# Kernel tuning notes

Hardware: AMD Instinct MI355X
Metric: run time of the kernel (lower is better)

## Reference

```python
import jax, jax.numpy as jnp
import numpy as np

PC_MIN = jnp.array([0.0, -40.0, -3.0], dtype=jnp.float32)
VS_TOP = jnp.array([0.4, 0.4, 4.0], dtype=jnp.float32)
VS_MED = jnp.array([0.2, 0.2, 2.0], dtype=jnp.float32)
VS_LOW = jnp.array([0.1, 0.1, 1.0], dtype=jnp.float32)
GRID_TOP = (176, 200, 1)
GRID_MED = (352, 400, 2)
GRID_LOW = (704, 800, 4)
EPS = 1e-3
FILL = np.iinfo(np.int32).max


def _bn(x, g, b):
    # training-mode BatchNorm1d over the point/voxel axis (naiveSyncBN1d, eps=1e-3)
    mu = jnp.mean(x, axis=0)
    var = jnp.var(x, axis=0)
    return (x - mu) * jax.lax.rsqrt(var + EPS) * g + b


def _decode(lin, gx, gy, gz):
    x = lin % gx
    r = lin // gx
    y = r % gy
    r = r // gy
    z = r % gz
    b = r // gz
    return b, x, y, z


def _vfe(pts, batch, vs, grid, W1, g1, b1, W2, g2, b2):
    # Dynamic voxelization + DynamicScatterVFE (cluster center + voxel center, 2 layers, scatter-mean).
    N = pts.shape[0]
    gx, gy, gz = grid
    xyz = pts[:, :3]
    coors = jnp.floor((xyz - PC_MIN) / vs).astype(jnp.int32)
    cx = jnp.clip(coors[:, 0], 0, gx - 1)
    cy = jnp.clip(coors[:, 1], 0, gy - 1)
    cz = jnp.clip(coors[:, 2], 0, gz - 1)
    lin = ((batch * gz + cz) * gy + cy) * gx + cx  # linear voxel id incl. batch
    uniq, inv = jnp.unique(lin, return_inverse=True, size=N, fill_value=FILL)
    valid = uniq != FILL
    cnt = jnp.maximum(jax.ops.segment_sum(jnp.ones((N,), pts.dtype), inv, num_segments=N), 1.0)
    seg_mean = lambda v: jax.ops.segment_sum(v, inv, num_segments=N) / cnt[:, None]
    f_cluster = xyz - seg_mean(xyz)[inv]                      # offset from per-voxel point mean
    centers = PC_MIN + (jnp.stack([cx, cy, cz], axis=1).astype(pts.dtype) + 0.5) * vs
    f_center = xyz - centers                                   # offset from voxel center
    feats = jnp.concatenate([pts, f_cluster, f_center], axis=1)  # [N, 10]
    h = jax.nn.relu(_bn(feats @ W1, g1, b1))
    h = jnp.concatenate([h, seg_mean(h)[inv]], axis=1)           # point feat || gathered voxel feat
    h = jax.nn.relu(_bn(h @ W2, g2, b2))
    vox = seg_mean(h)
    return jnp.where(valid[:, None], vox, 0.0), uniq, valid


def _merge(sub_feats, sub_uniq, sub_valid, top_uniq, sub_grid, factor):
    # find_coordinate_indices + scatter_v2(mode='avg'): mean of child voxel feats per parent voxel.
    b, x, y, z = _decode(sub_uniq, *sub_grid)
    gx, gy, gz = GRID_TOP
    parent = ((b * gz + z // factor) * gy + y // factor) * gx + x // factor
    M = top_uniq.shape[0]
    pos = jnp.clip(jnp.searchsorted(top_uniq, parent), 0, M - 1)
    found = sub_valid & (top_uniq[pos] == parent)
    seg = jnp.where(found, pos, M)  # unmatched/padding rows dropped into slot M
    s = jax.ops.segment_sum(sub_feats, seg, num_segments=M + 1)[:M]
    c = jax.ops.segment_sum(found.astype(sub_feats.dtype), seg, num_segments=M + 1)[:M]
    return s / jnp.maximum(c, 1.0)[:, None]


def setup_inputs() -> dict:
    key = jax.random.key(0)
    ks = jax.random.split(key, 12)
    N, B = 262144, 2
    x = jax.random.uniform(ks[0], (N, 1), jnp.float32, 0.0, 70.4)
    y = jax.random.uniform(ks[1], (N, 1), jnp.float32, -40.0, 40.0)
    z = jax.random.uniform(ks[2], (N, 1), jnp.float32, -3.0, 1.0)
    inten = jax.random.uniform(ks[3], (N, 1), jnp.float32)
    bcol = jnp.repeat(jnp.arange(B, dtype=jnp.float32), N // B)[:, None]
    points = jnp.concatenate([bcol, x, y, z, inten], axis=1)
    lin_w = lambda k, i, o: jax.random.normal(k, (i, o), jnp.float32) * (1.0 / np.sqrt(i))
    return dict(
        points=points, batch_size=2,
        W1_top=lin_w(ks[4], 10, 64), g1_top=jnp.ones(64), b1_top=jnp.zeros(64),
        W2_top=lin_w(ks[5], 128, 128), g2_top=jnp.ones(128), b2_top=jnp.zeros(128),
        W1_med=lin_w(ks[6], 10, 32), g1_med=jnp.ones(32), b1_med=jnp.zeros(32),
        W2_med=lin_w(ks[7], 64, 64), g2_med=jnp.ones(64), b2_med=jnp.zeros(64),
        W1_low=lin_w(ks[8], 10, 32), g1_low=jnp.ones(32), b1_low=jnp.zeros(32),
        W2_low=lin_w(ks[9], 64, 64), g2_low=jnp.ones(64), b2_low=jnp.zeros(64),
    )


def reference(points, batch_size, W1_top, g1_top, b1_top, W2_top, g2_top, b2_top,
              W1_med, g1_med, b1_med, W2_med, g2_med, b2_med,
              W1_low, g1_low, b1_low, W2_low, g2_low, b2_low):
    batch = points[:, 0].astype(jnp.int32)
    pts = points[:, 1:]
    vf, top_uniq, top_valid = _vfe(pts, batch, VS_TOP, GRID_TOP, W1_top, g1_top, b1_top, W2_top, g2_top, b2_top)
    mfeat, med_uniq, med_valid = _vfe(pts, batch, VS_MED, GRID_MED, W1_med, g1_med, b1_med, W2_med, g2_med, b2_med)
    lfeat, low_uniq, low_valid = _vfe(pts, batch, VS_LOW, GRID_LOW, W1_low, g1_low, b1_low, W2_low, g2_low, b2_low)
    med_mean = _merge(mfeat, med_uniq, med_valid, top_uniq, GRID_MED, 2)
    low_mean = _merge(lfeat, low_uniq, low_valid, top_uniq, GRID_LOW, 4)
    merged = jnp.where(top_valid[:, None], jnp.concatenate([med_mean, low_mean], axis=1), 0.0)
    b, x, y, z = _decode(top_uniq, *GRID_TOP)
    coors = jnp.where(top_valid[:, None], jnp.stack([b, z, y, x], axis=1), -1)
    return vf, merged, coors
```

## Files before the change

### kernel.cpp

```cpp
#include <hip/hip_runtime.h>
#include <cstdint>
#include <cstddef>

#define NPTS 262144
#define BLK 256
#define TGX 176
#define TGY 200
#define TGZ 1

#define G_TOPC 70400
#define G_MEDC 1126400
#define G_LOWC 4505600

#define SCAN_ITEMS 32
#define SCAN_CHUNK (BLK*SCAN_ITEMS)
#define NB_T 9
#define NB_M 138
#define NB_L 550
#define BO_T 0
#define BO_M 16
#define BO_L 160
#define NBVT (G_TOPC/BLK)
#define NBVM (NPTS/BLK)
#define NBVL (NPTS/BLK)

#define Y2B2 (NPTS/64)
#define ST1BLKS 256
#define NHT 4400
#define NHM 8192
#define NJT 8800
#define NJM 16384
#define NCL 275

typedef __attribute__((ext_vector_type(8))) short bf16x8;
typedef __attribute__((ext_vector_type(4))) float f32x4;

struct SP {
  const float4* srt; const int* jr; const float4* vm;
  const float* W1; const float* W2;
  const float* g1; const float* b1; const float* g2; const float* b2;
  const int* cnt; const int* uniq; const int* woff; const int* U;
  float* segt; float* part1; float* part2;
  float* coef1; float* coef2;
  unsigned short* Y2;
  float* hout;
  int C1; int segstride; int gx, gy, gz; float vx, vy, vz;
};

__device__ __forceinline__ unsigned short f2bf(float v) {
  unsigned u = __float_as_uint(v);
  u += 0x7FFFu + ((u >> 16) & 1u);
  return (unsigned short)(u >> 16);
}
__device__ __forceinline__ float bf2f(unsigned short h) {
  return __uint_as_float((unsigned)h << 16);
}

__device__ __forceinline__ void pcoords(float x, float y, float z,
    float vx, float vy, float vz, int gx, int gy, int gz,
    int& cx, int& cy, int& cz) {
  cx = (int)floorf((x - 0.0f)  / vx);
  cy = (int)floorf((y + 40.0f) / vy);
  cz = (int)floorf((z + 3.0f)  / vz);
  cx = min(max(cx, 0), gx - 1);
  cy = min(max(cy, 0), gy - 1);
  cz = min(max(cz, 0), gz - 1);
}

__device__ __forceinline__ int lin3(float b, float x, float y, float z,
    float vx, float vy, float vz, int gx, int gy, int gz) {
  int cx, cy, cz; pcoords(x, y, z, vx, vy, vz, gx, gy, gz, cx, cy, cz);
  return (((int)b * gz + cz) * gy + cy) * gx + cx;
}

__device__ __forceinline__ void build_f(float4 p, float4 vm,
    float vx, float vy, float vz, int gx, int gy, int gz, float* f) {
  int cx, cy, cz; pcoords(p.x, p.y, p.z, vx, vy, vz, gx, gy, gz, cx, cy, cz);
  f[0] = p.x; f[1] = p.y; f[2] = p.z; f[3] = p.w;
  f[4] = p.x - vm.x;
  f[5] = p.y - vm.y;
  f[6] = p.z - vm.z;
  f[7] = p.x - (0.0f   + (cx + 0.5f)*vx);
  f[8] = p.y - (-40.0f + (cy + 0.5f)*vy);
  f[9] = p.z - (-3.0f  + (cz + 0.5f)*vz);
}

__global__ __launch_bounds__(BLK) void k_count3(const float* __restrict__ pts,
    int* __restrict__ ct, int* __restrict__ cm, int* __restrict__ cl) {
  int i = blockIdx.x * BLK + threadIdx.x;
  if (i >= NPTS) return;
  float b = pts[i*5+0], x = pts[i*5+1], y = pts[i*5+2], z = pts[i*5+3];
  atomicAdd(&ct[lin3(b,x,y,z, 0.4f,0.4f,4.0f, 176,200,1)], 1);
  atomicAdd(&cm[lin3(b,x,y,z, 0.2f,0.2f,2.0f, 352,400,2)], 1);
  atomicAdd(&cl[lin3(b,x,y,z, 0.1f,0.1f,1.0f, 704,800,4)], 1);
}

__global__ __launch_bounds__(BLK) void k_scan1_all(const int* __restrict__ ct,
    const int* __restrict__ cm, const int* __restrict__ cl,
    int2* __restrict__ bsum) {
  int bid = blockIdx.x;
  const int* cnt; int G, bo, cb;
  if (bid < NB_T)            { cnt = ct; G = G_TOPC; bo = BO_T; cb = bid; }
  else if (bid < NB_T+NB_M)  { cnt = cm; G = G_MEDC; bo = BO_M; cb = bid - NB_T; }
  else                       { cnt = cl; G = G_LOWC; bo = BO_L; cb = bid - NB_T - NB_M; }
  int base = cb * SCAN_CHUNK + threadIdx.x * SCAN_ITEMS;
  int so = 0, sp = 0;
  #pragma unroll
  for (int k = 0; k < SCAN_ITEMS; k++) {
    int j = base + k;
    if (j < G) { int c = cnt[j]; if (c > 0) { so++; sp += c; } }
  }
  __shared__ int sho[BLK], shp[BLK];
  sho[threadIdx.x] = so; shp[threadIdx.x] = sp; __syncthreads();
  for (int off = BLK/2; off > 0; off >>= 1) {
    if (threadIdx.x < off) {
      sho[threadIdx.x] += sho[threadIdx.x + off];
      shp[threadIdx.x] += shp[threadIdx.x + off];
    }
    __syncthreads();
  }
  if (threadIdx.x == 0) { int2 v; v.x = sho[0]; v.y = shp[0]; bsum[bo + cb] = v; }
}

__device__ void scan_pass(int2* bsum, int off, int nb, int* U,
                          int* so, int* sp) {
  int t = threadIdx.x;
  int vo = 0, vp = 0;
  if (t < nb) { int2 v = bsum[off + t]; vo = v.x; vp = v.y; }
  so[t] = vo; sp[t] = vp; __syncthreads();
  for (int o = 1; o < 1024; o <<= 1) {
    int ao = (t >= o) ? so[t - o] : 0;
    int ap = (t >= o) ? sp[t - o] : 0;
    __syncthreads();
    so[t] += ao; sp[t] += ap;
    __syncthreads();
  }
  if (t < nb) { int2 e; e.x = so[t] - vo; e.y = sp[t] - vp; bsum[off + t] = e; }
  if (t == 0) *U = so[1023];
  __syncthreads();
}

__global__ __launch_bounds__(1024) void k_scan2_all(int2* __restrict__ bsum,
    int* __restrict__ Ut, int* __restrict__ Um, int* __restrict__ Ul) {
  __shared__ int so[1024], sp[1024];
  scan_pass(bsum, BO_T, NB_T, Ut, so, sp);
  scan_pass(bsum, BO_M, NB_M, Um, so, sp);
  scan_pass(bsum, BO_L, NB_L, Ul, so, sp);
}

__global__ __launch_bounds__(BLK) void k_scan3_all(const int* __restrict__ ct,
    const int* __restrict__ cm, const int* __restrict__ cl,
    const int2* __restrict__ bsum,
    int* __restrict__ rkt, int* __restrict__ rkm, int* __restrict__ rkl,
    int* __restrict__ uqt, int* __restrict__ uqm, int* __restrict__ uql,
    int* __restrict__ wot, int* __restrict__ wom, int* __restrict__ wol) {
  int bid = blockIdx.x;
  const int* cnt; int G, bo, cb; int *rank, *uniq, *woff;
  if (bid < NB_T)           { cnt=ct; G=G_TOPC; bo=BO_T; cb=bid;            rank=rkt; uniq=uqt; woff=wot; }
  else if (bid < NB_T+NB_M) { cnt=cm; G=G_MEDC; bo=BO_M; cb=bid-NB_T;       rank=rkm; uniq=uqm; woff=wom; }
  else                      { cnt=cl; G=G_LOWC; bo=BO_L; cb=bid-NB_T-NB_M;  rank=rkl; uniq=uql; woff=wol; }
  int base = cb * SCAN_CHUNK + threadIdx.x * SCAN_ITEMS;
  int so = 0, sp = 0;
  #pragma unroll
  for (int k = 0; k < SCAN_ITEMS; k++) {
    int j = base + k;
    if (j < G) { int c = cnt[j]; if (c > 0) { so++; sp += c; } }
  }
  __shared__ int sho[BLK], shp[BLK];
  sho[threadIdx.x] = so; shp[threadIdx.x] = sp; __syncthreads();
  for (int off = 1; off < BLK; off <<= 1) {
    int ao = (threadIdx.x >= off) ? sho[threadIdx.x - off] : 0;
    int ap = (threadIdx.x >= off) ? shp[threadIdx.x - off] : 0;
    __syncthreads();
    sho[threadIdx.x] += ao; shp[threadIdx.x] += ap;
    __syncthreads();
  }
  int2 bb = bsum[bo + cb];
  int ro = bb.x + sho[threadIdx.x] - so;
  int po = bb.y + shp[threadIdx.x] - sp;
  for (int k = 0; k < SCAN_ITEMS; k++) {
    int j = base + k;
    if (j < G) {
      int c = cnt[j];
      if (c > 0) { rank[j] = ro; uniq[ro] = j; woff[ro] = po; ro++; po += c; }
    }
  }
}

__global__ __launch_bounds__(BLK) void k_scatter3(const float* __restrict__ pts,
    const int* __restrict__ rkt, int* __restrict__ wot, float4* __restrict__ st, int* __restrict__ jt,
    const int* __restrict__ rkm, int* __restrict__ wom, float4* __restrict__ sm, int* __restrict__ jm,
    const int* __restrict__ rkl, int* __restrict__ wol, float4* __restrict__ sl, int* __restrict__ jl) {
  int i = blockIdx.x * BLK + threadIdx.x;
  if (i >= NPTS) return;
  float b = pts[i*5+0], x = pts[i*5+1], y = pts[i*5+2], z = pts[i*5+3], it = pts[i*5+4];
  float4 p; p.x = x; p.y = y; p.z = z; p.w = it;
  {
    int r = rkt[lin3(b,x,y,z, 0.4f,0.4f,4.0f, 176,200,1)];
    int j = atomicAdd(&wot[r], 1); st[j] = p; jt[j] = r;
  }
  {
    int r = rkm[lin3(b,x,y,z, 0.2f,0.2f,2.0f, 352,400,2)];
    int j = atomicAdd(&wom[r], 1); sm[j] = p; jm[j] = r;
  }
  {
    int r = rkl[lin3(b,x,y,z, 0.1f,0.1f,1.0f, 704,800,4)];
    int j = atomicAdd(&wol[r], 1); sl[j] = p; jl[j] = r;
  }
}

__global__ __launch_bounds__(BLK) void k_vox13(
    const float4* __restrict__ st, const int* __restrict__ uqt, const int* __restrict__ ct,
    const int* __restrict__ wot, const int* __restrict__ Ut, float4* __restrict__ vt,
    const float4* __restrict__ sm, const int* __restrict__ uqm, const int* __restrict__ cm,
    const int* __restrict__ wom, const int* __restrict__ Um, float4* __restrict__ vm,
    const float4* __restrict__ sl, const int* __restrict__ uql, const int* __restrict__ cl,
    const int* __restrict__ wol, const int* __restrict__ Ul, float4* __restrict__ vl) {
  int bid = blockIdx.x;
  const float4* srt; const int *uniq, *cnt, *woff, *Up; float4* vmean; int r;
  if (bid < NBVT)           { r = bid*BLK + threadIdx.x;           srt=st; uniq=uqt; cnt=ct; woff=wot; Up=Ut; vmean=vt; }
  else if (bid < NBVT+NBVM) { r = (bid-NBVT)*BLK + threadIdx.x;    srt=sm; uniq=uqm; cnt=cm; woff=wom; Up=Um; vmean=vm; }
  else                      { r = (bid-NBVT-NBVM)*BLK + threadIdx.x; srt=sl; uniq=uql; cnt=cl; woff=wol; Up=Ul; vmean=vl; }
  if (r >= *Up) return;
  int lin = uniq[r];
  int len = cnt[lin];
  int base = woff[r] - len;
  float sx = 0.f, sy = 0.f, sz = 0.f;
  for (int k = 0; k < len; k++) {
    float4 p = srt[base + k];
    sx += p.x; sy += p.y; sz += p.z;
  }
// ... 99 lines not shown
    }
    __syncthreads();
  }
  if (threadIdx.x == 0) {
    float mu  = ss[0] * (1.0f / NPTS);
    float var = sq[0] * (1.0f / NPTS) - mu*mu;
    float sc  = g[ch] * (1.0f / sqrtf(var + 1e-3f));
    coef[ch]     = sc;
    coef[C + ch] = fmaf(-mu, sc, b[ch]);
  }
}

__global__ __launch_bounds__(BLK) void k_partcoef2_all(SP a, SP b, SP c) {
  int bid = blockIdx.x; SP sp; int ch;
  if (bid < 128)      { sp = a; ch = bid; }
  else if (bid < 192) { sp = b; ch = bid - 128; }
  else                { sp = c; ch = bid - 192; }
  if (ch >= 2*sp.C1) return;
  partcoef_body(sp.part2, Y2B2, 2*sp.C1, ch, sp.g2, sp.b2, sp.coef2);
}

__global__ __launch_bounds__(BLK) void k_hsegT_all(SP a, SP b, SP c) {
  int bid = blockIdx.x; SP sp; int rb;
  if (bid < NHT)           { sp = a; rb = bid; }
  else if (bid < NHT+NHM)  { sp = b; rb = bid - NHT; }
  else                     { sp = c; rb = bid - NHT - NHM; }
  const int C1 = sp.C1;
  const int qsh = (C1 == 64) ? 4 : 3;
  __shared__ float w[640];
  __shared__ float sc[64], sb[64];
  for (int t = threadIdx.x; t < 10*C1; t += BLK) w[t] = sp.W1[t];
  for (int t = threadIdx.x; t < C1; t += BLK) { sc[t] = sp.coef1[t]; sb[t] = sp.coef1[C1 + t]; }
  __syncthreads();
  int tid = rb * BLK + threadIdx.x;
  int r = tid >> qsh;
  int q = tid & ((1 << qsh) - 1);
  if (r >= *sp.U) return;
  int lin = sp.uniq[r];
  int len = sp.cnt[lin];
  int base = sp.woff[r] - len;
  float4 vmn = sp.vm[r];
  int c0 = q * 4;
  float s0 = sc[c0+0], s1 = sc[c0+1], s2 = sc[c0+2], s3 = sc[c0+3];
  float o0 = sb[c0+0], o1 = sb[c0+1], o2 = sb[c0+2], o3 = sb[c0+3];
  float a0=0.f, a1=0.f, a2=0.f, a3=0.f;
  for (int k = 0; k < len; k++) {
    float4 p = sp.srt[base + k];
    float f[10];
    build_f(p, vmn, sp.vx, sp.vy, sp.vz, sp.gx, sp.gy, sp.gz, f);
    float y0=0.f, y1=0.f, y2=0.f, y3=0.f;
    #pragma unroll
    for (int d = 0; d < 10; d++) {
      float fv = f[d];
      const float* wr = &w[d*C1 + c0];
      y0 = fmaf(fv, wr[0], y0); y1 = fmaf(fv, wr[1], y1);
      y2 = fmaf(fv, wr[2], y2); y3 = fmaf(fv, wr[3], y3);
    }
    a0 += fmaxf(fmaf(y0, s0, o0), 0.f);
    a1 += fmaxf(fmaf(y1, s1, o1), 0.f);
    a2 += fmaxf(fmaf(y2, s2, o2), 0.f);
    a3 += fmaxf(fmaf(y3, s3, o3), 0.f);
  }
  float il = 1.0f / (float)len;
  sp.segt[(size_t)(c0+0)*sp.segstride + r] = a0*il;
  sp.segt[(size_t)(c0+1)*sp.segstride + r] = a1*il;
  sp.segt[(size_t)(c0+2)*sp.segstride + r] = a2*il;
  sp.segt[(size_t)(c0+3)*sp.segstride + r] = a3*il;
}

__global__ __launch_bounds__(BLK) void k_packB_all(
    const float* __restrict__ W2t_, unsigned short* __restrict__ Bt,
    const float* __restrict__ W2m_, unsigned short* __restrict__ Bm,
    const float* __restrict__ W2l_, unsigned short* __restrict__ Bl) {
  int bid = blockIdx.x;
  const float* W2; unsigned short* Bp; int C2, idx;
  if (bid < 64)      { W2 = W2t_; Bp = Bt; C2 = 128; idx = bid*BLK + threadIdx.x; }
  else if (bid < 80) { W2 = W2m_; Bp = Bm; C2 = 64;  idx = (bid-64)*BLK + threadIdx.x; }
  else               { W2 = W2l_; Bp = Bl; C2 = 64;  idx = (bid-80)*BLK + threadIdx.x; }
  if (idx >= C2*C2) return;
  int NCF = C2/16;
  int per_kb = NCF*512;
  int kb = idx / per_kb, rem = idx % per_kb;
  int cf = rem / 512, r2 = rem % 512;
  int lane = r2 >> 3, j = r2 & 7;
  int k = kb*32 + (lane >> 4)*8 + j;
  int col = cf*16 + (lane & 15);
  Bp[idx] = f2bf(W2[(size_t)k*C2 + col]);
}

template<int C1>
__device__ __forceinline__ void y2m_body(const SP& sp,
    const unsigned short* __restrict__ Bpk, int blk, unsigned short* Alds) {
  constexpr int K   = 2*C1;
  constexpr int C2  = 2*C1;
  constexpr int MT  = 64;
  constexpr int NKB = K / 32;
  constexpr int NCF = C2 / 16;
  constexpr int RB  = K * 2;
  const int tid  = threadIdx.x;
  const int base = blk * MT;

  {
    const int jst = tid & 63;
    const int qst = tid >> 6;
    int jr = sp.jr[base + jst];
    float4 p = sp.srt[base + jst];
    float4 vmn = sp.vm[jr];
    float fs[10];
    build_f(p, vmn, sp.vx, sp.vy, sp.vz, sp.gx, sp.gy, sp.gz, fs);
    const int k_lo = qst * (K/4);
    #pragma unroll
    for (int kk = 0; kk < K/8; kk++) {
      int k0 = k_lo + kk*2;
      float v0, v1;
      if (k0 < C1) {
        float y0 = 0.f, y1v = 0.f;
        #pragma unroll
        for (int d = 0; d < 10; d++) {
          y0  = fmaf(fs[d], sp.W1[d*C1 + k0],     y0);
          y1v = fmaf(fs[d], sp.W1[d*C1 + k0 + 1], y1v);
        }
        v0 = fmaxf(fmaf(y0,  sp.coef1[k0],   sp.coef1[C1 + k0]),   0.f);
        v1 = fmaxf(fmaf(y1v, sp.coef1[k0+1], sp.coef1[C1 + k0+1]), 0.f);
      } else {
        v0 = sp.segt[(size_t)(k0     - C1)*sp.segstride + jr];
        v1 = sp.segt[(size_t)(k0 + 1 - C1)*sp.segstride + jr];
      }
      unsigned u = (unsigned)f2bf(v0) | ((unsigned)f2bf(v1) << 16);
      int g  = k0 >> 3;
      int gp = g ^ (jst & 7);
      *(unsigned*)((char*)Alds + (size_t)jst*RB + gp*16 + (k0 & 7)*2) = u;
    }
  }
  __syncthreads();

  const int w    = tid >> 6;
  const int l    = tid & 63;
  const int rowf = l & 15;
  const int kg   = l >> 4;
  const int row  = w*16 + rowf;
  f32x4 acc[NCF];
  #pragma unroll
  for (int cf = 0; cf < NCF; cf++) acc[cf] = (f32x4){0.f, 0.f, 0.f, 0.f};
  #pragma unroll
  for (int kb = 0; kb < NKB; kb++) {
    int g  = kb*4 + kg;
    int gp = g ^ (row & 7);
    bf16x8 a = *(const bf16x8*)((const char*)Alds + (size_t)row*RB + gp*16);
    const bf16x8* bfr = (const bf16x8*)Bpk + (size_t)(kb*NCF)*64 + l;
    #pragma unroll
    for (int cf = 0; cf < NCF; cf++) {
// ... 35 lines not shown
    }
  }
  __syncthreads();
  for (int it = tid; it < MT*C2/8; it += BLK) {
    int r = (it*8) / C2;
    int c = (it*8) % C2;
    uint4 v = *(const uint4*)&D[it*8];
    *(uint4*)&sp.Y2[(size_t)(base + r)*C2 + c] = v;
  }
}

__global__ __launch_bounds__(BLK) void k_y2m_all(SP a, SP b, SP c,
    const unsigned short* __restrict__ Bt, const unsigned short* __restrict__ Bm,
    const unsigned short* __restrict__ Bl) {
  __shared__ unsigned short Alds[64*128];
  int bid = blockIdx.x;
  if (bid < Y2B2)        y2m_body<64>(a, Bt, bid, Alds);
  else if (bid < 2*Y2B2) y2m_body<32>(b, Bm, bid - Y2B2, Alds);
  else                   y2m_body<32>(c, Bl, bid - 2*Y2B2, Alds);
}

__global__ __launch_bounds__(BLK) void k_hseg2_all(SP a, SP b, SP c) {
  int bid = blockIdx.x; SP sp; int rb;
  if (bid < NJT)           { sp = a; rb = bid; }
  else if (bid < NJT+NJM)  { sp = b; rb = bid - NJT; }
  else                     { sp = c; rb = bid - NJT - NJM; }
  const int C = 2*sp.C1;
  const int qsh = (C == 128) ? 5 : 4;
  __shared__ float sc[128], sb[128];
  for (int t = threadIdx.x; t < C; t += BLK) { sc[t] = sp.coef2[t]; sb[t] = sp.coef2[C + t]; }
  __syncthreads();
  int tid = rb * BLK + threadIdx.x;
  int r = tid >> qsh;
  int q = tid & ((1 << qsh) - 1);
  if (r >= *sp.U) return;
  int lin = sp.uniq[r];
  int len = sp.cnt[lin];
  int base = sp.woff[r] - len;
  int c0 = q * 4;
  float s0 = sc[c0+0], s1 = sc[c0+1], s2 = sc[c0+2], s3 = sc[c0+3];
  float o0 = sb[c0+0], o1 = sb[c0+1], o2 = sb[c0+2], o3 = sb[c0+3];
  float a0=0.f, a1=0.f, a2=0.f, a3=0.f;
  const unsigned short* Yh = sp.Y2;
  for (int k = 0; k < len; k++) {
    ushort4 hv = *(const ushort4*)&Yh[(size_t)(base + k)*C + c0];
    a0 += fmaxf(fmaf(bf2f(hv.x), s0, o0), 0.f);
    a1 += fmaxf(fmaf(bf2f(hv.y), s1, o1), 0.f);
    a2 += fmaxf(fmaf(bf2f(hv.z), s2, o2), 0.f);
    a3 += fmaxf(fmaf(bf2f(hv.w), s3, o3), 0.f);
  }
  float il = 1.0f / (float)len;
  float4 o = {a0*il, a1*il, a2*il, a3*il};
  *(float4*)&sp.hout[(size_t)r*C + c0] = o;
}

__global__ __launch_bounds__(BLK) void k_clist_all(const int* __restrict__ tuniq,
    const int* __restrict__ Utp,
    const int* __restrict__ cnt_m, const int* __restrict__ rank_m,
    int* __restrict__ clist_m, int* __restrict__ mcnt_m,
    const int* __restrict__ cnt_l, const int* __restrict__ rank_l,
    int* __restrict__ clist_l, int* __restrict__ mcnt_l) {
  int bid = blockIdx.x;
  const int *scnt, *srank; int *clist, *mcnt;
  int gx, gy, gz, f, rb;
  if (bid < NCL) { scnt=cnt_m; srank=rank_m; clist=clist_m; mcnt=mcnt_m;
                   gx=352; gy=400; gz=2; f=2; rb=bid; }
  else           { scnt=cnt_l; srank=rank_l; clist=clist_l; mcnt=mcnt_l;
                   gx=704; gy=800; gz=4; f=4; rb=bid-NCL; }
  int r = rb * BLK + threadIdx.x;
  if (r >= *Utp) return;
  int lin = tuniq[r];
  int x = lin % TGX; int t = lin / TGX;
  int y = t % TGY;   int b = t / TGY;
  int m = 0;
  for (int cz = 0; cz < gz; cz++)
    for (int yy = y*f; yy < y*f + f; yy++)
      for (int xx = x*f; xx < x*f + f; xx++) {
        int cl = ((b*gz + cz)*gy + yy)*gx + xx;
        if (scnt[cl] > 0) clist[(size_t)r*64 + (m++)] = srank[cl];
      }
  mcnt[r] = m;
}

__global__ __launch_bounds__(BLK) void k_merge2_all(
    const float* __restrict__ vox_m, const int* __restrict__ clist_m,
    const int* __restrict__ mcnt_m,
    const float* __restrict__ vox_l, const int* __restrict__ clist_l,
    const int* __restrict__ mcnt_l,
    const int* __restrict__ Utp, float* __restrict__ mg) {
  int bid = blockIdx.x;
  const float* vox; const int *clist, *mcnt; int half, rb;
  if (bid < NHT) { vox=vox_m; clist=clist_m; mcnt=mcnt_m; half=0; rb=bid; }
  else           { vox=vox_l; clist=clist_l; mcnt=mcnt_l; half=64; rb=bid-NHT; }
  int idx = rb * BLK + threadIdx.x;
  int r = idx >> 4;
  int q = idx & 15;
  if (r >= *Utp) return;
  int m = mcnt[r];
  float a0=0.f, a1=0.f, a2=0.f, a3=0.f;
  for (int t = 0; t < m; t++) {
    int cr = clist[(size_t)r*64 + t];
    float4 v = *(const float4*)&vox[(size_t)cr*64 + q*4];
    a0 += v.x; a1 += v.y; a2 += v.z; a3 += v.w;
  }
  float inv = 1.0f / (float)max(m, 1);
  float4 o = {a0*inv, a1*inv, a2*inv, a3*inv};
  *(float4*)&mg[(size_t)r*128 + half + q*4] = o;
}

__global__ __launch_bounds__(BLK) void k_fin_all(const int* __restrict__ uniq,
    const int* __restrict__ Up, float* __restrict__ vf,
    float* __restrict__ mg, float* __restrict__ coors) {
  int idx = blockIdx.x * BLK + threadIdx.x;
  int r = idx >> 5;
  int q = idx & 31;
  if (r >= NPTS) return;
  int U = *Up;
  if (r >= U) {
    float4 z = {0.f, 0.f, 0.f, 0.f};
    *(float4*)&mg[(size_t)r*128 + q*4] = z;
    *(float4*)&vf[(size_t)r*128 + q*4] = z;
  }
  if (q == 0) {
    float4 co;
    if (r < U) {
      int lin = uniq[r];
      int x = lin % TGX; int t = lin / TGX;
      int y = t % TGY;   t /= TGY;
      int z = t % TGZ;   int b = t / TGZ;
      co.x = (float)b; co.y = (float)z; co.z = (float)y; co.w = (float)x;
    } else {
      co.x = -1.f; co.y = -1.f; co.z = -1.f; co.w = -1.f;
    }
    *(float4*)&coors[(size_t)r*4] = co;
  }
}
// ... 16 lines not shown
    return p;
  };
  int*    cnt_t   = (int*)alloc(((size_t)G_TOPC + G_MEDC + G_LOWC) * 4);
  int*    cnt_m   = cnt_t + G_TOPC;
  int*    cnt_l   = cnt_t + G_TOPC + G_MEDC;
  int*    rank_t  = (int*)alloc((size_t)G_TOPC * 4);
  int*    rank_m  = (int*)alloc((size_t)G_MEDC * 4);
  int*    rank_l  = (int*)alloc((size_t)G_LOWC * 4);
  int*    uniq_t  = (int*)alloc((size_t)G_TOPC * 4);
  int*    uniq_m  = (int*)alloc((size_t)NPTS * 4);
  int*    uniq_l  = (int*)alloc((size_t)NPTS * 4);
  int*    woff_t  = (int*)alloc((size_t)G_TOPC * 4);
  int*    woff_m  = (int*)alloc((size_t)NPTS * 4);
  int*    woff_l  = (int*)alloc((size_t)NPTS * 4);
  float4* srt_t   = (float4*)alloc((size_t)NPTS * 16);
  float4* srt_m   = (float4*)alloc((size_t)NPTS * 16);
  float4* srt_l   = (float4*)alloc((size_t)NPTS * 16);
  int*    jr_t    = (int*)alloc((size_t)NPTS * 4);
  int*    jr_m    = (int*)alloc((size_t)NPTS * 4);
  int*    jr_l    = (int*)alloc((size_t)NPTS * 4);
  float4* vm_t    = (float4*)alloc((size_t)G_TOPC * 16);
  float4* vm_m    = (float4*)alloc((size_t)NPTS * 16);
  float4* vm_l    = (float4*)alloc((size_t)NPTS * 16);
  float*  segt_t  = (float*)alloc((size_t)G_TOPC * 64 * 4);
  float*  segt_m  = (float*)alloc((size_t)NPTS * 32 * 4);
  float*  segt_l  = (float*)alloc((size_t)NPTS * 32 * 4);
  float*  vox_m   = (float*)alloc((size_t)NPTS * 64 * 4);
  float*  vox_l   = (float*)alloc((size_t)NPTS * 64 * 4);
  unsigned short* Y2h_t = (unsigned short*)alloc((size_t)NPTS * 128 * 2);
  unsigned short* Y2h_m = (unsigned short*)alloc((size_t)NPTS * 64 * 2);
  unsigned short* Y2h_l = (unsigned short*)alloc((size_t)NPTS * 64 * 2);
  unsigned short* Bpk_t = (unsigned short*)alloc(16384 * 2);
  unsigned short* Bpk_m = (unsigned short*)alloc(4096 * 2);
  unsigned short* Bpk_l = (unsigned short*)alloc(4096 * 2);
  int*    clist_m = (int*)alloc((size_t)G_TOPC * 64 * 4);
  int*    clist_l = (int*)alloc((size_t)G_TOPC * 64 * 4);
  int*    mcnt_m  = (int*)alloc((size_t)G_TOPC * 4);
  int*    mcnt_l  = (int*)alloc((size_t)G_TOPC * 4);
  float*  part1_t = (float*)alloc((size_t)ST1BLKS * 128 * 4);
  float*  part1_m = (float*)alloc((size_t)ST1BLKS * 128 * 4);
  float*  part1_l = (float*)alloc((size_t)ST1BLKS * 128 * 4);
  float*  part2_t = (float*)alloc((size_t)Y2B2 * 256 * 4);
  float*  part2_m = (float*)alloc((size_t)Y2B2 * 128 * 4);
  float*  part2_l = (float*)alloc((size_t)Y2B2 * 128 * 4);
  float*  coef    = (float*)alloc(6 * 256 * 4);
  int2*   bsum    = (int2*)alloc(1024 * 8);
  int*    Ut      = (int*)alloc(64);
  int*    Um      = (int*)alloc(64);
  int*    Ul      = (int*)alloc(64);
// ... 19 lines not shown
      s.g2 = (const float*)d_in[12]; s.b2 = (const float*)d_in[13];
      s.cnt = cnt_m; s.uniq = uniq_m; s.woff = woff_m; s.U = Um;
      s.segt = segt_m; s.part1 = part1_m; s.part2 = part2_m;
      s.coef1 = coef + 2*256; s.coef2 = coef + 3*256;
      s.Y2 = Y2h_m; s.hout = vox_m;
      s.C1 = 32; s.segstride = NPTS;
      s.gx = 352; s.gy = 400; s.gz = 2; s.vx = 0.2f; s.vy = 0.2f; s.vz = 2.0f;
    } else {
      s.srt = srt_l; s.jr = jr_l; s.vm = vm_l;
      s.W1 = (const float*)d_in[14]; s.g1 = (const float*)d_in[15];
      s.b1 = (const float*)d_in[16]; s.W2 = (const float*)d_in[17];
      s.g2 = (const float*)d_in[18]; s.b2 = (const float*)d_in[19];
      s.cnt = cnt_l; s.uniq = uniq_l; s.woff = woff_l; s.U = Ul;
      s.segt = segt_l; s.part1 = part1_l; s.part2 = part2_l;
      s.coef1 = coef + 4*256; s.coef2 = coef + 5*256;
      s.Y2 = Y2h_l; s.hout = vox_l;
      s.C1 = 32; s.segstride = NPTS;
      s.gx = 704; s.gy = 800; s.gz = 4; s.vx = 0.1f; s.vy = 0.1f; s.vz = 1.0f;
    }
    return s;
  };
  SP spT = mkSP(0), spM = mkSP(1), spL = mkSP(2);

  k_packB_all<<<96, BLK, 0, stream>>>((const float*)d_in[5], Bpk_t,
      (const float*)d_in[11], Bpk_m, (const float*)d_in[17], Bpk_l);

  (void)hipMemsetAsync(cnt_t, 0, ((size_t)G_TOPC + G_MEDC + G_LOWC) * 4, stream);
  k_count3<<<NPTS/BLK, BLK, 0, stream>>>(pts, cnt_t, cnt_m, cnt_l);
  k_scan1_all<<<NB_T + NB_M + NB_L, BLK, 0, stream>>>(cnt_t, cnt_m, cnt_l, bsum);
  k_scan2_all<<<1, 1024, 0, stream>>>(bsum, Ut, Um, Ul);
  k_scan3_all<<<NB_T + NB_M + NB_L, BLK, 0, stream>>>(cnt_t, cnt_m, cnt_l, bsum,
      rank_t, rank_m, rank_l, uniq_t, uniq_m, uniq_l, woff_t, woff_m, woff_l);
  k_clist_all<<<2*NCL, BLK, 0, stream>>>(uniq_t, Ut,
      cnt_m, rank_m, clist_m, mcnt_m, cnt_l, rank_l, clist_l, mcnt_l);
  k_scatter3<<<NPTS/BLK, BLK, 0, stream>>>(pts,
      rank_t, woff_t, srt_t, jr_t,
      rank_m, woff_m, srt_m, jr_m,
      rank_l, woff_l, srt_l, jr_l);
  k_vox13<<<NBVT + NBVM + NBVL, BLK, 0, stream>>>(
      srt_t, uniq_t, cnt_t, woff_t, Ut, vm_t,
      srt_m, uniq_m, cnt_m, woff_m, Um, vm_m,
      srt_l, uniq_l, cnt_l, woff_l, Ul, vm_l);

  k_fmom_all<<<3*ST1BLKS, BLK, 0, stream>>>(spT, spM, spL);
  k_mcoef_all<<<3, BLK, 0, stream>>>(spT, spM, spL);
  k_hsegT_all<<<NHT + 2*NHM, BLK, 0, stream>>>(spT, spM, spL);
  k_y2m_all<<<3*Y2B2, BLK, 0, stream>>>(spT, spM, spL, Bpk_t, Bpk_m, Bpk_l);
  k_partcoef2_all<<<256, BLK, 0, stream>>>(spT, spM, spL);
  k_hseg2_all<<<NJT + 2*NJM, BLK, 0, stream>>>(spT, spM, spL);

  k_merge2_all<<<2*NHT, BLK, 0, stream>>>(vox_m, clist_m, mcnt_m,
      vox_l, clist_l, mcnt_l, Ut, mg);
  k_fin_all<<<(NPTS*32)/BLK, BLK, 0, stream>>>(uniq_t, Ut, vf, mg, co);
}
```

Baseline: 683.7 us.

## Fuse small kernels, wave-shuffle scan, bf16 segment buffer, 8-wide segment loops

Merges several small launches into combined kernels: weight packing with counting, the child-list build with scatter, and merge with finalize. The 1024-thread shared-memory scan is replaced by a three-wave shuffle scan. The per-voxel segment-mean buffer is stored as bf16, halving its traffic, and the per-voxel segment loops now handle 8 channels per thread with wider loads. These changes aim to cut launch overhead and memory traffic. The bf16 storage of the segment mean changes rounding slightly, and the fused merge/finalize assumes no ordering dependency between its two halves.

```diff
diff --git a/kernel.cpp b/kernel.cpp
--- a/kernel.cpp
+++ b/kernel.cpp
@@ -26,10 +26,12 @@
 
 #define Y2B2 (NPTS/64)
 #define ST1BLKS 256
-#define NHT 4400
-#define NHM 8192
-#define NJT 8800
-#define NJM 16384
+#define NHT2 2200
+#define NHM2 4096
+#define NJT2 4400
+#define NJM2 8192
+#define NMG 4400
+#define FINB 32768
 #define NCL 275
 
 typedef __attribute__((ext_vector_type(8))) short bf16x8;
@@ -40,7 +42,8 @@
   const float* W1; const float* W2;
   const float* g1; const float* b1; const float* g2; const float* b2;
   const int* cnt; const int* uniq; const int* woff; const int* U;
-  float* segt; float* part1; float* part2;
+  unsigned short* segt;
+  float* part1; float* part2;
   float* coef1; float* coef2;
   unsigned short* Y2;
   float* hout;
@@ -85,14 +88,34 @@
   f[9] = p.z - (-3.0f  + (cz + 0.5f)*vz);
 }
 
-__global__ __launch_bounds__(BLK) void k_count3(const float* __restrict__ pts,
-    int* __restrict__ ct, int* __restrict__ cm, int* __restrict__ cl) {
-  int i = blockIdx.x * BLK + threadIdx.x;
-  if (i >= NPTS) return;
-  float b = pts[i*5+0], x = pts[i*5+1], y = pts[i*5+2], z = pts[i*5+3];
-  atomicAdd(&ct[lin3(b,x,y,z, 0.4f,0.4f,4.0f, 176,200,1)], 1);
-  atomicAdd(&cm[lin3(b,x,y,z, 0.2f,0.2f,2.0f, 352,400,2)], 1);
-  atomicAdd(&cl[lin3(b,x,y,z, 0.1f,0.1f,1.0f, 704,800,4)], 1);
+__global__ __launch_bounds__(BLK) void k_count3pack(const float* __restrict__ pts,
+    int* __restrict__ ct, int* __restrict__ cm, int* __restrict__ cl,
+    const float* __restrict__ W2t_, unsigned short* __restrict__ Bt,
+    const float* __restrict__ W2m_, unsigned short* __restrict__ Bm,
+    const float* __restrict__ W2l_, unsigned short* __restrict__ Bl) {
+  int bid = blockIdx.x;
+  if (bid < NPTS/BLK) {
+    int i = bid * BLK + threadIdx.x;
+    float b = pts[i*5+0], x = pts[i*5+1], y = pts[i*5+2], z = pts[i*5+3];
+    atomicAdd(&ct[lin3(b,x,y,z, 0.4f,0.4f,4.0f, 176,200,1)], 1);
+    atomicAdd(&cm[lin3(b,x,y,z, 0.2f,0.2f,2.0f, 352,400,2)], 1);
+    atomicAdd(&cl[lin3(b,x,y,z, 0.1f,0.1f,1.0f, 704,800,4)], 1);
+    return;
+  }
+  int pb = bid - NPTS/BLK;
+  const float* W2; unsigned short* Bp; int C2, idx;
+  if (pb < 64)      { W2 = W2t_; Bp = Bt; C2 = 128; idx = pb*BLK + threadIdx.x; }
+  else if (pb < 80) { W2 = W2m_; Bp = Bm; C2 = 64;  idx = (pb-64)*BLK + threadIdx.x; }
+  else              { W2 = W2l_; Bp = Bl; C2 = 64;  idx = (pb-80)*BLK + threadIdx.x; }
+  if (idx >= C2*C2) return;
+  int NCF = C2/16;
+  int per_kb = NCF*512;
+  int kb = idx / per_kb, rem = idx % per_kb;
+  int cf = rem / 512, r2 = rem % 512;
+  int lane = r2 >> 3, j = r2 & 7;
+  int k = kb*32 + (lane >> 4)*8 + j;
+  int col = cf*16 + (lane & 15);
+  Bp[idx] = f2bf(W2[(size_t)k*C2 + col]);
 }
 
 __global__ __launch_bounds__(BLK) void k_scan1_all(const int* __restrict__ ct,
@@ -122,30 +145,40 @@
   if (threadIdx.x == 0) { int2 v; v.x = sho[0]; v.y = shp[0]; bsum[bo + cb] = v; }
 }
 
-__device__ void scan_pass(int2* bsum, int off, int nb, int* U,
-                          int* so, int* sp) {
-  int t = threadIdx.x;
-  int vo = 0, vp = 0;
-  if (t < nb) { int2 v = bsum[off + t]; vo = v.x; vp = v.y; }
-  so[t] = vo; sp[t] = vp; __syncthreads();
-  for (int o = 1; o < 1024; o <<= 1) {
-    int ao = (t >= o) ? so[t - o] : 0;
-    int ap = (t >= o) ? sp[t - o] : 0;
-    __syncthreads();
-    so[t] += ao; sp[t] += ap;
-    __syncthreads();
-  }
-  if (t < nb) { int2 e; e.x = so[t] - vo; e.y = sp[t] - vp; bsum[off + t] = e; }
-  if (t == 0) *U = so[1023];
-  __syncthreads();
-}
-
-__global__ __launch_bounds__(1024) void k_scan2_all(int2* __restrict__ bsum,
+__global__ __launch_bounds__(192) void k_scan2_all(int2* __restrict__ bsum,
     int* __restrict__ Ut, int* __restrict__ Um, int* __restrict__ Ul) {
-  __shared__ int so[1024], sp[1024];
-  scan_pass(bsum, BO_T, NB_T, Ut, so, sp);
-  scan_pass(bsum, BO_M, NB_M, Um, so, sp);
-  scan_pass(bsum, BO_L, NB_L, Ul, so, sp);
+  int wv = threadIdx.x >> 6;
+  int lane = threadIdx.x & 63;
+  int off, nb; int* U;
+  if (wv == 0)      { off = BO_T; nb = NB_T; U = Ut; }
+  else if (wv == 1) { off = BO_M; nb = NB_M; U = Um; }
+  else              { off = BO_L; nb = NB_L; U = Ul; }
+  const int IPL = 9;
+  int eo[IPL], ep[IPL];
+  int accO = 0, accP = 0;
+  #pragma unroll
+  for (int k = 0; k < IPL; k++) {
+    int idx = lane*IPL + k;
+    int2 t = {0, 0};
+    if (idx < nb) t = bsum[off + idx];
+    eo[k] = accO; ep[k] = accP;
+    accO += t.x; accP += t.y;
+  }
+  int xo = accO, xp = accP;
+  #pragma unroll
+  for (int d = 1; d < 64; d <<= 1) {
+    int to = __shfl_up(xo, d);
+    int tp = __shfl_up(xp, d);
+    if (lane >= d) { xo += to; xp += tp; }
+  }
+  int baseO = xo - accO, baseP = xp - accP;
+  #pragma unroll
+  for (int k = 0; k < IPL; k++) {
+    int idx = lane*IPL + k;
+    if (idx < nb) { int2 e; e.x = baseO + eo[k]; e.y = baseP + ep[k]; bsum[off + idx] = e; }
+  }
+  int tot = __shfl(xo, 63);
+  if (lane == 0) *U = tot;
 }
 
 __global__ __launch_bounds__(BLK) void k_scan3_all(const int* __restrict__ ct,
@@ -187,26 +220,54 @@
   }
 }
 
-__global__ __launch_bounds__(BLK) void k_scatter3(const float* __restrict__ pts,
+__global__ __launch_bounds__(BLK) void k_scatclist(const float* __restrict__ pts,
     const int* __restrict__ rkt, int* __restrict__ wot, float4* __restrict__ st, int* __restrict__ jt,
     const int* __restrict__ rkm, int* __restrict__ wom, float4* __restrict__ sm, int* __restrict__ jm,
-    const int* __restrict__ rkl, int* __restrict__ wol, float4* __restrict__ sl, int* __restrict__ jl) {
-  int i = blockIdx.x * BLK + threadIdx.x;
-  if (i >= NPTS) return;
-  float b = pts[i*5+0], x = pts[i*5+1], y = pts[i*5+2], z = pts[i*5+3], it = pts[i*5+4];
-  float4 p; p.x = x; p.y = y; p.z = z; p.w = it;
-  {
-    int r = rkt[lin3(b,x,y,z, 0.4f,0.4f,4.0f, 176,200,1)];
-    int j = atomicAdd(&wot[r], 1); st[j] = p; jt[j] = r;
-  }
-  {
-    int r = rkm[lin3(b,x,y,z, 0.2f,0.2f,2.0f, 352,400,2)];
-    int j = atomicAdd(&wom[r], 1); sm[j] = p; jm[j] = r;
-  }
-  {
-    int r = rkl[lin3(b,x,y,z, 0.1f,0.1f,1.0f, 704,800,4)];
-    int j = atomicAdd(&wol[r], 1); sl[j] = p; jl[j] = r;
-  }
+    const int* __restrict__ rkl, int* __restrict__ wol, float4* __restrict__ sl, int* __restrict__ jl,
+    const int* __restrict__ tuniq, const int* __restrict__ Utp,
+    const int* __restrict__ cnt_m, const int* __restrict__ rank_m,
+    int* __restrict__ clist_m, int* __restrict__ mcnt_m,
+    const int* __restrict__ cnt_l, const int* __restrict__ rank_l,
+    int* __restrict__ clist_l, int* __restrict__ mcnt_l) {
+  int bid = blockIdx.x;
+  if (bid < NPTS/BLK) {
+    int i = bid * BLK + threadIdx.x;
+    float b = pts[i*5+0], x = pts[i*5+1], y = pts[i*5+2], z = pts[i*5+3], it = pts[i*5+4];
+    float4 p; p.x = x; p.y = y; p.z = z; p.w = it;
+    {
+      int r = rkt[lin3(b,x,y,z, 0.4f,0.4f,4.0f, 176,200,1)];
+      int j = atomicAdd(&wot[r], 1); st[j] = p; jt[j] = r;
+    }
+    {
+      int r = rkm[lin3(b,x,y,z, 0.2f,0.2f,2.0f, 352,400,2)];
+      int j = atomicAdd(&wom[r], 1); sm[j] = p; jm[j] = r;
+    }
+    {
+      int r = rkl[lin3(b,x,y,z, 0.1f,0.1f,1.0f, 704,800,4)];
+      int j = atomicAdd(&wol[r], 1); sl[j] = p; jl[j] = r;
+    }
+    return;
+  }
+  int cb = bid - NPTS/BLK;
+  const int *scnt, *srank; int *clist, *mcnt;
+  int gx, gy, gz, f, rb;
+  if (cb < NCL) { scnt=cnt_m; srank=rank_m; clist=clist_m; mcnt=mcnt_m;
+                  gx=352; gy=400; gz=2; f=2; rb=cb; }
+  else          { scnt=cnt_l; srank=rank_l; clist=clist_l; mcnt=mcnt_l;
+                  gx=704; gy=800; gz=4; f=4; rb=cb-NCL; }
+  int r = rb * BLK + threadIdx.x;
+  if (r >= *Utp) return;
+  int lin = tuniq[r];
+  int x = lin % TGX; int t = lin / TGX;
+  int y = t % TGY;   int b = t / TGY;
+  int m = 0;
+  for (int cz = 0; cz < gz; cz++)
+    for (int yy = y*f; yy < y*f + f; yy++)
+      for (int xx = x*f; xx < x*f + f; xx++) {
+        int cl = ((b*gz + cz)*gy + yy)*gx + xx;
+        if (scnt[cl] > 0) clist[(size_t)r*64 + (m++)] = srank[cl];
+      }
+  mcnt[r] = m;
 }
 
 __global__ __launch_bounds__(BLK) void k_vox13(
@@ -352,11 +413,11 @@
 
 __global__ __launch_bounds__(BLK) void k_hsegT_all(SP a, SP b, SP c) {
   int bid = blockIdx.x; SP sp; int rb;
-  if (bid < NHT)           { sp = a; rb = bid; }
-  else if (bid < NHT+NHM)  { sp = b; rb = bid - NHT; }
-  else                     { sp = c; rb = bid - NHT - NHM; }
+  if (bid < NHT2)           { sp = a; rb = bid; }
+  else if (bid < NHT2+NHM2) { sp = b; rb = bid - NHT2; }
+  else                      { sp = c; rb = bid - NHT2 - NHM2; }
   const int C1 = sp.C1;
-  const int qsh = (C1 == 64) ? 4 : 3;
+  const int qsh = (C1 == 64) ? 3 : 2;
   __shared__ float w[640];
   __shared__ float sc[64], sb[64];
   for (int t = threadIdx.x; t < 10*C1; t += BLK) w[t] = sp.W1[t];
@@ -370,52 +431,29 @@
   int len = sp.cnt[lin];
   int base = sp.woff[r] - len;
   float4 vmn = sp.vm[r];
-  int c0 = q * 4;
-  float s0 = sc[c0+0], s1 = sc[c0+1], s2 = sc[c0+2], s3 = sc[c0+3];
-  float o0 = sb[c0+0], o1 = sb[c0+1], o2 = sb[c0+2], o3 = sb[c0+3];
-  float a0=0.f, a1=0.f, a2=0.f, a3=0.f;
+  int c0 = q * 8;
+  float s[8], o[8], acc[8];
+  #pragma unroll
+  for (int e = 0; e < 8; e++) { s[e] = sc[c0+e]; o[e] = sb[c0+e]; acc[e] = 0.f; }
   for (int k = 0; k < len; k++) {
     float4 p = sp.srt[base + k];
     float f[10];
     build_f(p, vmn, sp.vx, sp.vy, sp.vz, sp.gx, sp.gy, sp.gz, f);
-    float y0=0.f, y1=0.f, y2=0.f, y3=0.f;
+    float y[8] = {0,0,0,0,0,0,0,0};
     #pragma unroll
     for (int d = 0; d < 10; d++) {
       float fv = f[d];
       const float* wr = &w[d*C1 + c0];
-      y0 = fmaf(fv, wr[0], y0); y1 = fmaf(fv, wr[1], y1);
-      y2 = fmaf(fv, wr[2], y2); y3 = fmaf(fv, wr[3], y3);
-    }
-    a0 += fmaxf(fmaf(y0, s0, o0), 0.f);
-    a1 += fmaxf(fmaf(y1, s1, o1), 0.f);
-    a2 += fmaxf(fmaf(y2, s2, o2), 0.f);
-    a3 += fmaxf(fmaf(y3, s3, o3), 0.f);
+      #pragma unroll
+      for (int e = 0; e < 8; e++) y[e] = fmaf(fv, wr[e], y[e]);
+    }
+    #pragma unroll
+    for (int e = 0; e < 8; e++) acc[e] += fmaxf(fmaf(y[e], s[e], o[e]), 0.f);
   }
   float il = 1.0f / (float)len;
-  sp.segt[(size_t)(c0+0)*sp.segstride + r] = a0*il;
-  sp.segt[(size_t)(c0+1)*sp.segstride + r] = a1*il;
-  sp.segt[(size_t)(c0+2)*sp.segstride + r] = a2*il;
-  sp.segt[(size_t)(c0+3)*sp.segstride + r] = a3*il;
-}
-
-__global__ __launch_bounds__(BLK) void k_packB_all(
-    const float* __restrict__ W2t_, unsigned short* __restrict__ Bt,
-    const float* __restrict__ W2m_, unsigned short* __restrict__ Bm,
-    const float* __restrict__ W2l_, unsigned short* __restrict__ Bl) {
-  int bid = blockIdx.x;
-  const float* W2; unsigned short* Bp; int C2, idx;
-  if (bid < 64)      { W2 = W2t_; Bp = Bt; C2 = 128; idx = bid*BLK + threadIdx.x; }
-  else if (bid < 80) { W2 = W2m_; Bp = Bm; C2 = 64;  idx = (bid-64)*BLK + threadIdx.x; }
-  else               { W2 = W2l_; Bp = Bl; C2 = 64;  idx = (bid-80)*BLK + threadIdx.x; }
-  if (idx >= C2*C2) return;
-  int NCF = C2/16;
-  int per_kb = NCF*512;
-  int kb = idx / per_kb, rem = idx % per_kb;
-  int cf = rem / 512, r2 = rem % 512;
-  int lane = r2 >> 3, j = r2 & 7;
-  int k = kb*32 + (lane >> 4)*8 + j;
-  int col = cf*16 + (lane & 15);
-  Bp[idx] = f2bf(W2[(size_t)k*C2 + col]);
+  #pragma unroll
+  for (int e = 0; e < 8; e++)
+    sp.segt[(size_t)(c0+e)*sp.segstride + r] = f2bf(acc[e]*il);
 }
 
 template<int C1>
@@ -442,7 +480,7 @@
     #pragma unroll
     for (int kk = 0; kk < K/8; kk++) {
       int k0 = k_lo + kk*2;
-      float v0, v1;
+      unsigned u;
       if (k0 < C1) {
         float y0 = 0.f, y1v = 0.f;
         #pragma unroll
@@ -450,13 +488,14 @@
           y0  = fmaf(fs[d], sp.W1[d*C1 + k0],     y0);
           y1v = fmaf(fs[d], sp.W1[d*C1 + k0 + 1], y1v);
         }
-        v0 = fmaxf(fmaf(y0,  sp.coef1[k0],   sp.coef1[C1 + k0]),   0.f);
-        v1 = fmaxf(fmaf(y1v, sp.coef1[k0+1], sp.coef1[C1 + k0+1]), 0.f);
+        float v0 = fmaxf(fmaf(y0,  sp.coef1[k0],   sp.coef1[C1 + k0]),   0.f);
+        float v1 = fmaxf(fmaf(y1v, sp.coef1[k0+1], sp.coef1[C1 + k0+1]), 0.f);
+        u = (unsigned)f2bf(v0) | ((unsigned)f2bf(v1) << 16);
       } else {
-        v0 = sp.segt[(size_t)(k0     - C1)*sp.segstride + jr];
-        v1 = sp.segt[(size_t)(k0 + 1 - C1)*sp.segstride + jr];
+        unsigned s0 = sp.segt[(size_t)(k0     - C1)*sp.segstride + jr];
+        unsigned s1 = sp.segt[(size_t)(k0 + 1 - C1)*sp.segstride + jr];
+        u = s0 | (s1 << 16);
       }
-      unsigned u = (unsigned)f2bf(v0) | ((unsigned)f2bf(v1) << 16);
       int g  = k0 >> 3;
       int gp = g ^ (jst & 7);
       *(unsigned*)((char*)Alds + (size_t)jst*RB + gp*16 + (k0 & 7)*2) = u;
@@ -538,11 +577,11 @@
 
 __global__ __launch_bounds__(BLK) void k_hseg2_all(SP a, SP b, SP c) {
   int bid = blockIdx.x; SP sp; int rb;
-  if (bid < NJT)           { sp = a; rb = bid; }
-  else if (bid < NJT+NJM)  { sp = b; rb = bid - NJT; }
-  else                     { sp = c; rb = bid - NJT - NJM; }
+  if (bid < NJT2)           { sp = a; rb = bid; }
+  else if (bid < NJT2+NJM2) { sp = b; rb = bid - NJT2; }
+  else                      { sp = c; rb = bid - NJT2 - NJM2; }
   const int C = 2*sp.C1;
-  const int qsh = (C == 128) ? 5 : 4;
+  const int qsh = (C == 128) ? 4 : 3;
   __shared__ float sc[128], sb[128];
   for (int t = threadIdx.x; t < C; t += BLK) { sc[t] = sp.coef2[t]; sb[t] = sp.coef2[C + t]; }
   __syncthreads();
@@ -553,81 +592,58 @@
   int lin = sp.uniq[r];
   int len = sp.cnt[lin];
   int base = sp.woff[r] - len;
-  int c0 = q * 4;
-  float s0 = sc[c0+0], s1 = sc[c0+1], s2 = sc[c0+2], s3 = sc[c0+3];
-  float o0 = sb[c0+0], o1 = sb[c0+1], o2 = sb[c0+2], o3 = sb[c0+3];
-  float a0=0.f, a1=0.f, a2=0.f, a3=0.f;
+  int c0 = q * 8;
+  float s[8], o[8], acc[8];
+  #pragma unroll
+  for (int e = 0; e < 8; e++) { s[e] = sc[c0+e]; o[e] = sb[c0+e]; acc[e] = 0.f; }
   const unsigned short* Yh = sp.Y2;
   for (int k = 0; k < len; k++) {
-    ushort4 hv = *(const ushort4*)&Yh[(size_t)(base + k)*C + c0];
-    a0 += fmaxf(fmaf(bf2f(hv.x), s0, o0), 0.f);
-    a1 += fmaxf(fmaf(bf2f(hv.y), s1, o1), 0.f);
-    a2 += fmaxf(fmaf(bf2f(hv.z), s2, o2), 0.f);
-    a3 += fmaxf(fmaf(bf2f(hv.w), s3, o3), 0.f);
+    uint4 hv = *(const uint4*)&Yh[(size_t)(base + k)*C + c0];
+    unsigned uu[4] = {hv.x, hv.y, hv.z, hv.w};
+    #pragma unroll
+    for (int j = 0; j < 4; j++) {
+      float lo = __uint_as_float(uu[j] << 16);
+      float hi = __uint_as_float(uu[j] & 0xFFFF0000u);
+      acc[2*j+0] += fmaxf(fmaf(lo, s[2*j+0], o[2*j+0]), 0.f);
+      acc[2*j+1] += fmaxf(fmaf(hi, s[2*j+1], o[2*j+1]), 0.f);
+    }
   }
   float il = 1.0f / (float)len;
-  float4 o = {a0*il, a1*il, a2*il, a3*il};
-  *(float4*)&sp.hout[(size_t)r*C + c0] = o;
-}
-
-__global__ __launch_bounds__(BLK) void k_clist_all(const int* __restrict__ tuniq,
-    const int* __restrict__ Utp,
-    const int* __restrict__ cnt_m, const int* __restrict__ rank_m,
-    int* __restrict__ clist_m, int* __restrict__ mcnt_m,
-    const int* __restrict__ cnt_l, const int* __restrict__ rank_l,
-    int* __restrict__ clist_l, int* __restrict__ mcnt_l) {
-  int bid = blockIdx.x;
-  const int *scnt, *srank; int *clist, *mcnt;
-  int gx, gy, gz, f, rb;
-  if (bid < NCL) { scnt=cnt_m; srank=rank_m; clist=clist_m; mcnt=mcnt_m;
-                   gx=352; gy=400; gz=2; f=2; rb=bid; }
-  else           { scnt=cnt_l; srank=rank_l; clist=clist_l; mcnt=mcnt_l;
-                   gx=704; gy=800; gz=4; f=4; rb=bid-NCL; }
-  int r = rb * BLK + threadIdx.x;
-  if (r >= *Utp) return;
-  int lin = tuniq[r];
-  int x = lin % TGX; int t = lin / TGX;
-  int y = t % TGY;   int b = t / TGY;
-  int m = 0;
-  for (int cz = 0; cz < gz; cz++)
-    for (int yy = y*f; yy < y*f + f; yy++)
-      for (int xx = x*f; xx < x*f + f; xx++) {
-        int cl = ((b*gz + cz)*gy + yy)*gx + xx;
-        if (scnt[cl] > 0) clist[(size_t)r*64 + (m++)] = srank[cl];
-      }
-  mcnt[r] = m;
-}
-
-__global__ __launch_bounds__(BLK) void k_merge2_all(
+  float4 o0 = {acc[0]*il, acc[1]*il, acc[2]*il, acc[3]*il};
+  float4 o1 = {acc[4]*il, acc[5]*il, acc[6]*il, acc[7]*il};
+  *(float4*)&sp.hout[(size_t)r*C + c0]     = o0;
+  *(float4*)&sp.hout[(size_t)r*C + c0 + 4] = o1;
+}
+
+__global__ __launch_bounds__(BLK) void k_mergefin(
     const float* __restrict__ vox_m, const int* __restrict__ clist_m,
     const int* __restrict__ mcnt_m,
     const float* __restrict__ vox_l, const int* __restrict__ clist_l,
     const int* __restrict__ mcnt_l,
-    const int* __restrict__ Utp, float* __restrict__ mg) {
+    const int* __restrict__ uniq, const int* __restrict__ Up,
+    float* __restrict__ vf, float* __restrict__ mg, float* __restrict__ coors) {
   int bid = blockIdx.x;
-  const float* vox; const int *clist, *mcnt; int half, rb;
-  if (bid < NHT) { vox=vox_m; clist=clist_m; mcnt=mcnt_m; half=0; rb=bid; }
-  else           { vox=vox_l; clist=clist_l; mcnt=mcnt_l; half=64; rb=bid-NHT; }
-  int idx = rb * BLK + threadIdx.x;
-  int r = idx >> 4;
-  int q = idx & 15;
-  if (r >= *Utp) return;
-  int m = mcnt[r];
-  float a0=0.f, a1=0.f, a2=0.f, a3=0.f;
-  for (int t = 0; t < m; t++) {
-    int cr = clist[(size_t)r*64 + t];
-    float4 v = *(const float4*)&vox[(size_t)cr*64 + q*4];
-    a0 += v.x; a1 += v.y; a2 += v.z; a3 += v.w;
-  }
-  float inv = 1.0f / (float)max(m, 1);
-  float4 o = {a0*inv, a1*inv, a2*inv, a3*inv};
-  *(float4*)&mg[(size_t)r*128 + half + q*4] = o;
-}
-
-__global__ __launch_bounds__(BLK) void k_fin_all(const int* __restrict__ uniq,
-    const int* __restrict__ Up, float* __restrict__ vf,
-    float* __restrict__ mg, float* __restrict__ coors) {
-  int idx = blockIdx.x * BLK + threadIdx.x;
+  if (bid < 2*NMG) {
+    const float* vox; const int *clist, *mcnt; int half, rb;
+    if (bid < NMG) { vox=vox_m; clist=clist_m; mcnt=mcnt_m; half=0; rb=bid; }
+    else           { vox=vox_l; clist=clist_l; mcnt=mcnt_l; half=64; rb=bid-NMG; }
+    int idx = rb * BLK + threadIdx.x;
+    int r = idx >> 4;
+    int q = idx & 15;
+    if (r >= *Up) return;
+    int m = mcnt[r];
+    float a0=0.f, a1=0.f, a2=0.f, a3=0.f;
+    for (int t = 0; t < m; t++) {
+      int cr = clist[(size_t)r*64 + t];
+      float4 v = *(const float4*)&vox[(size_t)cr*64 + q*4];
+      a0 += v.x; a1 += v.y; a2 += v.z; a3 += v.w;
+    }
+    float inv = 1.0f / (float)max(m, 1);
+    float4 o = {a0*inv, a1*inv, a2*inv, a3*inv};
+    *(float4*)&mg[(size_t)r*128 + half + q*4] = o;
+    return;
+  }
+  int idx = (bid - 2*NMG) * BLK + threadIdx.x;
   int r = idx >> 5;
   int q = idx & 31;
   if (r >= NPTS) return;
@@ -690,9 +706,9 @@
   float4* vm_t    = (float4*)alloc((size_t)G_TOPC * 16);
   float4* vm_m    = (float4*)alloc((size_t)NPTS * 16);
   float4* vm_l    = (float4*)alloc((size_t)NPTS * 16);
-  float*  segt_t  = (float*)alloc((size_t)G_TOPC * 64 * 4);
-  float*  segt_m  = (float*)alloc((size_t)NPTS * 32 * 4);
-  float*  segt_l  = (float*)alloc((size_t)NPTS * 32 * 4);
+  unsigned short* segt_t = (unsigned short*)alloc((size_t)G_TOPC * 64 * 2);
+  unsigned short* segt_m = (unsigned short*)alloc((size_t)NPTS * 32 * 2);
+  unsigned short* segt_l = (unsigned short*)alloc((size_t)NPTS * 32 * 2);
   float*  vox_m   = (float*)alloc((size_t)NPTS * 64 * 4);
   float*  vox_l   = (float*)alloc((size_t)NPTS * 64 * 4);
   unsigned short* Y2h_t = (unsigned short*)alloc((size_t)NPTS * 128 * 2);
@@ -758,21 +774,19 @@
   };
   SP spT = mkSP(0), spM = mkSP(1), spL = mkSP(2);
 
-  k_packB_all<<<96, BLK, 0, stream>>>((const float*)d_in[5], Bpk_t,
-      (const float*)d_in[11], Bpk_m, (const float*)d_in[17], Bpk_l);
-
   (void)hipMemsetAsync(cnt_t, 0, ((size_t)G_TOPC + G_MEDC + G_LOWC) * 4, stream);
-  k_count3<<<NPTS/BLK, BLK, 0, stream>>>(pts, cnt_t, cnt_m, cnt_l);
+  k_count3pack<<<NPTS/BLK + 96, BLK, 0, stream>>>(pts, cnt_t, cnt_m, cnt_l,
+      (const float*)d_in[5], Bpk_t, (const float*)d_in[11], Bpk_m,
+      (const float*)d_in[17], Bpk_l);
   k_scan1_all<<<NB_T + NB_M + NB_L, BLK, 0, stream>>>(cnt_t, cnt_m, cnt_l, bsum);
-  k_scan2_all<<<1, 1024, 0, stream>>>(bsum, Ut, Um, Ul);
+  k_scan2_all<<<1, 192, 0, stream>>>(bsum, Ut, Um, Ul);
   k_scan3_all<<<NB_T + NB_M + NB_L, BLK, 0, stream>>>(cnt_t, cnt_m, cnt_l, bsum,
       rank_t, rank_m, rank_l, uniq_t, uniq_m, uniq_l, woff_t, woff_m, woff_l);
-  k_clist_all<<<2*NCL, BLK, 0, stream>>>(uniq_t, Ut,
-      cnt_m, rank_m, clist_m, mcnt_m, cnt_l, rank_l, clist_l, mcnt_l);
-  k_scatter3<<<NPTS/BLK, BLK, 0, stream>>>(pts,
+  k_scatclist<<<NPTS/BLK + 2*NCL, BLK, 0, stream>>>(pts,
       rank_t, woff_t, srt_t, jr_t,
       rank_m, woff_m, srt_m, jr_m,
-      rank_l, woff_l, srt_l, jr_l);
+      rank_l, woff_l, srt_l, jr_l,
+      uniq_t, Ut, cnt_m, rank_m, clist_m, mcnt_m, cnt_l, rank_l, clist_l, mcnt_l);
   k_vox13<<<NBVT + NBVM + NBVL, BLK, 0, stream>>>(
       srt_t, uniq_t, cnt_t, woff_t, Ut, vm_t,
       srt_m, uniq_m, cnt_m, woff_m, Um, vm_m,
@@ -780,12 +794,11 @@
 
   k_fmom_all<<<3*ST1BLKS, BLK, 0, stream>>>(spT, spM, spL);
   k_mcoef_all<<<3, BLK, 0, stream>>>(spT, spM, spL);
-  k_hsegT_all<<<NHT + 2*NHM, BLK, 0, stream>>>(spT, spM, spL);
+  k_hsegT_all<<<NHT2 + 2*NHM2, BLK, 0, stream>>>(spT, spM, spL);
   k_y2m_all<<<3*Y2B2, BLK, 0, stream>>>(spT, spM, spL, Bpk_t, Bpk_m, Bpk_l);
   k_partcoef2_all<<<256, BLK, 0, stream>>>(spT, spM, spL);
-  k_hseg2_all<<<NJT + 2*NJM, BLK, 0, stream>>>(spT, spM, spL);
-
-  k_merge2_all<<<2*NHT, BLK, 0, stream>>>(vox_m, clist_m, mcnt_m,
-      vox_l, clist_l, mcnt_l, Ut, mg);
-  k_fin_all<<<(NPTS*32)/BLK, BLK, 0, stream>>>(uniq_t, Ut, vf, mg, co);
-}
+  k_hseg2_all<<<NJT2 + 2*NJM2, BLK, 0, stream>>>(spT, spM, spL);
+
+  k_mergefin<<<2*NMG + FINB, BLK, 0, stream>>>(vox_m, clist_m, mcnt_m,
+      vox_l, clist_l, mcnt_l, uniq_t, Ut, vf, mg, co);
+}
```

Result: faster. 609.4 us (median of 2 runs) (-10.9%).
